# Optimization experiments

Hardware: AMD Instinct MI355X
Metric: run time of the kernel (lower is better)

## Reference

```python
import jax, jax.numpy as jnp
import numpy as np

WIN = (2, 4, 4)
SHIFT = (1, 2, 2)
NUM_HEADS = 8
LN_EPS = 1e-5


def _rel_pos_index(ws):
    wt, wh, ww = ws
    coords = np.stack(np.meshgrid(np.arange(wt), np.arange(wh), np.arange(ww), indexing='ij'))
    cf = coords.reshape(3, -1)                      # [3, N]
    rel = cf[:, :, None] - cf[:, None, :]           # [3, N, N]
    rel = rel.transpose(1, 2, 0).copy()             # [N, N, 3]
    rel[..., 0] += wt - 1
    rel[..., 1] += wh - 1
    rel[..., 2] += ww - 1
    rel[..., 0] *= (2 * wh - 1) * (2 * ww - 1)
    rel[..., 1] *= 2 * ww - 1
    return rel.sum(-1)                              # [N, N] int

REL_IDX = _rel_pos_index(WIN)


def _layer_norm(x, w, b):
    mu = jnp.mean(x, axis=-1, keepdims=True)
    var = jnp.mean(jnp.square(x - mu), axis=-1, keepdims=True)
    return (x - mu) * jax.lax.rsqrt(var + LN_EPS) * w + b


def setup_inputs() -> dict:
    key = jax.random.key(0)
    ks = jax.random.split(key, 8)
    C, Cm = 256, 1024
    inp = {
        'x': jax.random.normal(ks[0], (2, 16, 64, 64, C), jnp.float32),
        'norm1_w': jnp.ones((C,), jnp.float32),
        'norm1_b': jnp.zeros((C,), jnp.float32),
        'qkv_w': jax.random.normal(ks[1], (C, 3 * C), jnp.float32) * 0.02,
        'qkv_b': jnp.zeros((3 * C,), jnp.float32),
        'proj_w': jax.random.normal(ks[2], (C, C), jnp.float32) * 0.02,
        'proj_b': jnp.zeros((C,), jnp.float32),
        'rel_bias_table': jax.random.normal(ks[3], (147, NUM_HEADS), jnp.float32) * 0.02,
        'norm2_w': jnp.ones((C,), jnp.float32),
        'norm2_b': jnp.zeros((C,), jnp.float32),
        'mlp_w1': jax.random.normal(ks[4], (C, Cm), jnp.float32) * 0.02,
        'mlp_b1': jnp.zeros((Cm,), jnp.float32),
        'mlp_w2': jax.random.normal(ks[5], (Cm, C), jnp.float32) * 0.02,
        'mlp_b2': jnp.zeros((C,), jnp.float32),
    }
    return inp


def reference(x, norm1_w, norm1_b, qkv_w, qkv_b, proj_w, proj_b,
              rel_bias_table, norm2_w, norm2_b, mlp_w1, mlp_b1, mlp_w2, mlp_b2):
    B, T, H, W, C = x.shape
    wT, wH, wW = WIN
    nh = NUM_HEADS
    d = C // nh
    scale = d ** (-0.5)
    N = wT * wH * wW

    shortcut = x
    h = _layer_norm(x, norm1_w, norm1_b)
    # cyclic shift (no attention mask is applied in the original block)
    h = jnp.roll(h, shift=(-SHIFT[0], -SHIFT[1], -SHIFT[2]), axis=(1, 2, 3))
    # window partition -> [B*nW, N, C]
    h = h.reshape(B, T // wT, wT, H // wH, wH, W // wW, wW, C)
    h = h.transpose(0, 1, 3, 5, 2, 4, 6, 7).reshape(-1, N, C)
    B_ = h.shape[0]

    qkv = (h @ qkv_w + qkv_b).reshape(B_, N, 3, nh, d).transpose(2, 0, 3, 1, 4)
    q, k, v = qkv[0] * scale, qkv[1], qkv[2]          # [B_, nh, N, d]
    attn = jnp.einsum('bhnd,bhmd->bhnm', q, k)        # [B_, nh, N, N]
    bias = rel_bias_table[REL_IDX].transpose(2, 0, 1)  # [nh, N, N]
    attn = jax.nn.softmax(attn + bias[None], axis=-1)
    o = jnp.einsum('bhnm,bhmd->bhnd', attn, v)
    o = o.transpose(0, 2, 1, 3).reshape(B_, N, C)
    o = o @ proj_w + proj_b

    # window reverse -> [B, T, H, W, C]
    o = o.reshape(B, T // wT, H // wH, W // wW, wT, wH, wW, C)
    o = o.transpose(0, 1, 4, 2, 5, 3, 6, 7).reshape(B, T, H, W, C)
    o = jnp.roll(o, shift=SHIFT, axis=(1, 2, 3))

    x = shortcut + o
    m = _layer_norm(x, norm2_w, norm2_b)
    m = jax.nn.gelu(m @ mlp_w1 + mlp_b1, approximate=False) @ mlp_w2 + mlp_b2
    return x + m
```

## Files before the change

### kernel.cpp

```cpp
#include <hip/hip_runtime.h>
#include <hip/hip_bf16.h>
#include <cstdint>
#include <cstddef>

typedef __attribute__((ext_vector_type(8)))  short  s16x8;
typedef __attribute__((ext_vector_type(4)))  float  fp32x4;
typedef __attribute__((ext_vector_type(16))) float  fp32x16;
typedef __attribute__((ext_vector_type(4)))  unsigned short u16x4;

static __device__ __forceinline__ float bf2f(unsigned short u) {
    union { unsigned int i; float f; } v; v.i = ((unsigned int)u) << 16; return v.f;
}
static __device__ __forceinline__ unsigned short f2bf(float f) {
    __hip_bfloat16 h = __float2bfloat16(f);
    return __builtin_bit_cast(unsigned short, h);
}

static __device__ __forceinline__ fp32x16 mfma32(s16x8 a, s16x8 b, fp32x16 c) {
    return __builtin_amdgcn_mfma_f32_32x32x16_bf16(a, b, c, 0, 0, 0);
}
static __device__ __forceinline__ fp32x4 mfma16(s16x8 a, s16x8 b, fp32x4 c) {
    return __builtin_amdgcn_mfma_f32_16x16x32_bf16(a, b, c, 0, 0, 0);
}

static __device__ __forceinline__ float wave_sum(float v) {
#pragma unroll
    for (int off = 32; off > 0; off >>= 1) v += __shfl_xor(v, off, 64);
    return v;
}

#define NTOK   131072
#define CDIM   256

__global__ void prep_kernel(const float* __restrict__ qkv_w, const float* __restrict__ proj_w,
                            const float* __restrict__ w1,    const float* __restrict__ w2,
                            const float* __restrict__ rel,
                            unsigned short* __restrict__ qkvT, unsigned short* __restrict__ projT,
                            unsigned short* __restrict__ w1T,  unsigned short* __restrict__ w2T,
                            float* __restrict__ btab) {
    int id = blockIdx.x * 256 + threadIdx.x;
    if (id < 196608) {
        int n = id >> 8, k = id & 255;
        qkvT[id] = f2bf(qkv_w[k * 768 + n]);
    } else if (id < 262144) {
        int e = id - 196608; int n = e >> 8, k = e & 255;
        projT[e] = f2bf(proj_w[k * 256 + n]);
    } else if (id < 524288) {
        int e = id - 262144; int n = e >> 8, k = e & 255;
        w1T[e] = f2bf(w1[k * 1024 + n]);
    } else if (id < 786432) {
        int e = id - 524288; int n = e >> 10, k = e & 1023;
        w2T[e] = f2bf(w2[k * 256 + n]);
    } else {
        int e = id - 786432;
        int h = e >> 10, rem = e & 1023, n = rem >> 5, m = rem & 31;
        int tn = n >> 4, hn = (n >> 2) & 3, wn = n & 3;
        int tm = m >> 4, hm = (m >> 2) & 3, wm = m & 3;
        int ridx = (tn - tm + 1) * 49 + (hn - hm + 3) * 7 + (wn - wm + 3);
        btab[e] = rel[ridx * 8 + h];
    }
}

template <int MODE>
__global__ __launch_bounds__(256) void ln_kernel(const float* __restrict__ in,
                                                 const float* __restrict__ w,
                                                 const float* __restrict__ b,
                                                 unsigned short* __restrict__ out) {
    int tid = threadIdx.x, lane = tid & 63, wid = tid >> 6;
    long r = (long)blockIdx.x * 4 + wid;
    long src;
    if (MODE == 0) {
        int n = (int)(r & 31); int win = (int)(r >> 5);
        int b_ = win >> 11, tw = (win >> 8) & 7, hw = (win >> 4) & 15, ww = win & 15;
        int ti = n >> 4, hi = (n >> 2) & 3, wi = n & 3;
        int t = tw * 2 + ti, hh = hw * 4 + hi, wv = ww * 4 + wi;
        int ts = (t + 1) & 15, hs = (hh + 2) & 63, wsd = (wv + 2) & 63;
        src = ((long)((b_ * 16 + ts) * 64 + hs)) * 64 + wsd;
    } else {
        src = r;
    }
    float4 v = *(const float4*)&in[src * CDIM + lane * 4];
    float vv[4] = {v.x, v.y, v.z, v.w};
    float s = vv[0] + vv[1] + vv[2] + vv[3];
    s = wave_sum(s);
    float mean = s * (1.0f / 256.0f);
    float q = vv[0]*vv[0] + vv[1]*vv[1] + vv[2]*vv[2] + vv[3]*vv[3];
    q = wave_sum(q);
    float var = q * (1.0f / 256.0f) - mean * mean;
    float rstd = rsqrtf(var + 1e-5f);
    int c0 = lane * 4;
    u16x4 o;
#pragma unroll
    for (int j = 0; j < 4; ++j)
        o[j] = f2bf((vv[j] - mean) * rstd * w[c0 + j] + b[c0 + j]);
    *(u16x4*)&out[r * CDIM + c0] = o;
}

template <int K, int EPI, int NS, int NX>
__global__ __launch_bounds__(512) void gemm256(const unsigned short* __restrict__ A,
                                               const unsigned short* __restrict__ Bt,
                                               const float* __restrict__ bias,
                                               float* __restrict__ outf,
                                               unsigned short* __restrict__ outb,
                                               const float* __restrict__ resid) {
    extern __shared__ unsigned short lds[];
    const int tid = threadIdx.x;
    const int lane = tid & 63, wid = tid >> 6;
    const int wm = wid >> 2, wn = wid & 3;
    constexpr int NWG = NX * 512;
    constexpr int CPX = NWG / 8;
    const int bid = blockIdx.x;
    const int wg = (bid & 7) * CPX + (bid >> 3);
    const int n0 = (wg % NX) * 256;
    const size_t m0 = (size_t)(wg / NX) * 256;
    constexpr int NK = K / 64;

    fp32x4 acc[8][4] = {};

    auto stage = [&](int kt, int buf) {
#pragma unroll
        for (int i = 0; i < 4; ++i) {
            int L = i * 512 + tid;
            int r = L >> 3, c = L & 7;
            int sc = c ^ (r & 7);
            const unsigned short* ga = A + (m0 + r) * K + kt * 64 + sc * 8;
            __builtin_amdgcn_global_load_lds(
                (const __attribute__((address_space(1))) void*)ga,
                (__attribute__((address_space(3))) void*)(lds + buf * 16384 + L * 8),
                16, 0, 0);
            const unsigned short* gb = Bt + (size_t)(n0 + r) * K + kt * 64 + sc * 8;
            __builtin_amdgcn_global_load_lds(
                (const __attribute__((address_space(1))) void*)gb,
                (__attribute__((address_space(3))) void*)(lds + 32768 + buf * 16384 + L * 8),
                16, 0, 0);
        }
    };

    stage(0, 0);
    __syncthreads();
    for (int kt = 0; kt < NK; ++kt) {
        if (kt + 1 < NK) stage(kt + 1, (kt + 1) & 1);
        const unsigned short* As = lds + (kt & 1) * 16384;
        const unsigned short* Bs = lds + 32768 + (kt & 1) * 16384;
#pragma unroll
        for (int q = 0; q < 4; ++q) {
            const int qm = q >> 1, qn = q & 1;
            s16x8 a[4][2], b[2][2];
#pragma unroll
            for (int m = 0; m < 4; ++m)
#pragma unroll
                for (int ks = 0; ks < 2; ++ks) {
                    int row = wm * 128 + qm * 64 + m * 16 + (lane & 15);
                    int j = ks * 4 + (lane >> 4);
                    a[m][ks] = *(const s16x8*)(As + row * 64 + ((j ^ (row & 7)) << 3));
                }
#pragma unroll
            for (int n = 0; n < 2; ++n)
#pragma unroll
                for (int ks = 0; ks < 2; ++ks) {
                    int row = wn * 64 + qn * 32 + n * 16 + (lane & 15);
                    int j = ks * 4 + (lane >> 4);
                    b[n][ks] = *(const s16x8*)(Bs + row * 64 + ((j ^ (row & 7)) << 3));
                }
#pragma unroll
            for (int ks = 0; ks < 2; ++ks)
#pragma unroll
                for (int m = 0; m < 4; ++m)
#pragma unroll
                    for (int n = 0; n < 2; ++n)
                        acc[qm * 4 + m][qn * 2 + n] =
                            mfma16(a[m][ks], b[n][ks], acc[qm * 4 + m][qn * 2 + n]);
        }
        __syncthreads();
    }

    float bv[4];
#pragma unroll
    for (int n = 0; n < 4; ++n) bv[n] = bias[n0 + wn * 64 + n * 16 + (lane & 15)];

#pragma unroll
    for (int m = 0; m < 8; ++m) {
#pragma unroll
        for (int rg = 0; rg < 4; ++rg) {
            int row_t = wm * 128 + m * 16 + ((lane >> 4) << 2) + rg;
            size_t gr = m0 + row_t;
            size_t dst = 0;
            if (EPI == 1) {
                int win = (int)(gr >> 5), n_ = (int)(gr & 31);
                int b_ = win >> 11, tw = (win >> 8) & 7, hw = (win >> 4) & 15, ww = win & 15;
                int ti = n_ >> 4, hi = (n_ >> 2) & 3, wi = n_ & 3;
                int t = tw * 2 + ti, hh = hw * 4 + hi, wv = ww * 4 + wi;
                int ts = (t + 1) & 15, hs = (hh + 2) & 63, wsd = (wv + 2) & 63;
                dst = ((size_t)((b_ * 16 + ts) * 64 + hs)) * 64 + wsd;
            }
#pragma unroll
            for (int n = 0; n < 4; ++n) {
                int gc = n0 + wn * 64 + n * 16 + (lane & 15);
                float v = acc[m][n][rg] + bv[n];
                if (EPI == 0) {
                    outb[gr * NS + gc] = f2bf(v);
                } else if (EPI == 1) {
                    outf[dst * CDIM + gc] = resid[dst * CDIM + gc] + v;
                } else if (EPI == 2) {
                    float g = 0.5f * v * (1.0f + erff(v * 0.70710678118654752f));
                    outb[gr * NS + gc] = f2bf(g);
                } else {
                    outf[gr * NS + gc] += v;
                }
            }
        }
    }
}

__global__ __launch_bounds__(256) void attn_kernel(const unsigned short* __restrict__ qkv,
                                                   const float* __restrict__ btab,
                                                   unsigned short* __restrict__ obuf) {
    __shared__ unsigned short sP[4][1280];
    __shared__ unsigned short sVt[4][1280];
    int tid = threadIdx.x, lane = tid & 63, wid = tid >> 6;
    int task = blockIdx.x * 4 + wid;
    int win = task >> 3, hh = task & 7;
    const unsigned short* base = qkv + (size_t)win * 32 * 768 + hh * 32;
    int q = lane & 31, h = lane >> 5;

    s16x8 v0 = *(const s16x8*)(base + 512 + q * 768 + h * 16);
    s16x8 v1 = *(const s16x8*)(base + 512 + q * 768 + h * 16 + 8);
#pragma unroll
    for (int j = 0; j < 8; ++j) {
        sVt[wid][(h * 16 + j) * 40 + q]     = (unsigned short)v0[j];
        sVt[wid][(h * 16 + 8 + j) * 40 + q] = (unsigned short)v1[j];
    }

    s16x8 aq0 = *(const s16x8*)(base + q * 768 + h * 8);
    s16x8 aq1 = *(const s16x8*)(base + q * 768 + 16 + h * 8);
    s16x8 bk0 = *(const s16x8*)(base + 256 + q * 768 + h * 8);
    s16x8 bk1 = *(const s16x8*)(base + 256 + q * 768 + 16 + h * 8);
    fp32x16 S = {0.0f};
    S = mfma32(aq0, bk0, S);
    S = mfma32(aq1, bk1, S);

    const float scale = 0.17677669529663687f;
    float pr[16];
#pragma unroll
    for (int r = 0; r < 16; ++r) {
        int row = (r & 3) + 8 * (r >> 2) + 4 * h;
        float bvv = btab[(hh * 32 + row) * 32 + q];
        pr[r] = S[r] * scale + bvv;
    }
#pragma unroll
    for (int r = 0; r < 16; ++r) {
        float mx = pr[r];
#pragma unroll
        for (int off = 16; off > 0; off >>= 1) mx = fmaxf(mx, __shfl_xor(mx, off, 64));
        float e = __expf(pr[r] - mx);
        float sm = e;
#pragma unroll
        for (int off = 16; off > 0; off >>= 1) sm += __shfl_xor(sm, off, 64);
        pr[r] = e * __builtin_amdgcn_rcpf(sm);
    }
#pragma unroll
    for (int r = 0; r < 16; ++r) {
        int row = (r & 3) + 8 * (r >> 2) + 4 * h;
        sP[wid][row * 40 + q] = f2bf(pr[r]);
    }
    __syncthreads();

    s16x8 pa0 = *(const s16x8*)&sP[wid][q * 40 + h * 8];
    s16x8 pa1 = *(const s16x8*)&sP[wid][q * 40 + 16 + h * 8];
    s16x8 vb0 = *(const s16x8*)&sVt[wid][q * 40 + h * 8];
    s16x8 vb1 = *(const s16x8*)&sVt[wid][q * 40 + 16 + h * 8];
    fp32x16 O = {0.0f};
    O = mfma32(pa0, vb0, O);
    O = mfma32(pa1, vb1, O);
#pragma unroll
    for (int r = 0; r < 16; ++r) {
        int row = (r & 3) + 8 * (r >> 2) + 4 * h;
        obuf[((size_t)win * 32 + row) * 256 + hh * 32 + q] = f2bf(O[r]);
    }
}

extern "C" void kernel_launch(void* const* d_in, const int* in_sizes, int n_in,
                              void* d_out, int out_size, void* d_ws, size_t ws_size,
                              hipStream_t stream) {
    const float* x      = (const float*)d_in[0];
    const float* n1w    = (const float*)d_in[1];
    const float* n1b    = (const float*)d_in[2];
    const float* qkv_w  = (const float*)d_in[3];
    const float* qkv_b  = (const float*)d_in[4];
    const float* proj_w = (const float*)d_in[5];
    const float* proj_b = (const float*)d_in[6];
    const float* rel    = (const float*)d_in[7];
    const float* n2w    = (const float*)d_in[8];
    const float* n2b    = (const float*)d_in[9];
    const float* w1     = (const float*)d_in[10];
    const float* b1     = (const float*)d_in[11];
    const float* w2     = (const float*)d_in[12];
    const float* b2     = (const float*)d_in[13];
    float* out = (float*)d_out;

    char* ws = (char*)d_ws;
    unsigned short* hwin = (unsigned short*)ws;
    unsigned short* big  = (unsigned short*)(ws + 67108864);
    char* wreg = ws + 67108864 + 268435456;
    unsigned short* qkvT  = (unsigned short*)(wreg);
    unsigned short* projT = (unsigned short*)(wreg + 393216);
    unsigned short* w1T   = (unsigned short*)(wreg + 524288);
    unsigned short* w2T   = (unsigned short*)(wreg + 1048576);
    float*          btab  = (float*)(wreg + 1572864);

    prep_kernel<<<3104, 256, 0, stream>>>(qkv_w, proj_w, w1, w2, rel, qkvT, projT, w1T, w2T, btab);

    ln_kernel<0><<<NTOK / 4, 256, 0, stream>>>(x, n1w, n1b, hwin);

    gemm256<256, 0, 768, 3><<<1536, 512, 131072, stream>>>(hwin, qkvT, qkv_b, nullptr, big, nullptr);

    attn_kernel<<<8192, 256, 0, stream>>>(big, btab, hwin);

    gemm256<256, 1, 256, 1><<<512, 512, 131072, stream>>>(hwin, projT, proj_b, out, nullptr, x);

    ln_kernel<1><<<NTOK / 4, 256, 0, stream>>>(out, n2w, n2b, hwin);

    gemm256<256, 2, 1024, 4><<<2048, 512, 131072, stream>>>(hwin, w1T, b1, nullptr, big, nullptr);

    gemm256<1024, 3, 256, 1><<<512, 512, 131072, stream>>>(big, w2T, b2, out, nullptr, nullptr);
}
```

Before: 597.8 us.

## Fuse LayerNorm2 into projection GEMM epilogue and use tanh-form GELU

```diff
diff --git a/kernel.cpp b/kernel.cpp
--- a/kernel.cpp
+++ b/kernel.cpp
@@ -27,6 +27,11 @@
 #pragma unroll
     for (int off = 32; off > 0; off >>= 1) v += __shfl_xor(v, off, 64);
     return v;
+}
+
+static __device__ __forceinline__ float gelu_f(float u) {
+    float t = u * (1.0f + 0.044715f * u * u) * 1.595769122f;
+    return u * (1.0f / (1.0f + __expf(-t)));
 }
 
 #define NTOK   131072
@@ -61,24 +66,19 @@
     }
 }
 
-template <int MODE>
 __global__ __launch_bounds__(256) void ln_kernel(const float* __restrict__ in,
                                                  const float* __restrict__ w,
                                                  const float* __restrict__ b,
                                                  unsigned short* __restrict__ out) {
     int tid = threadIdx.x, lane = tid & 63, wid = tid >> 6;
     long r = (long)blockIdx.x * 4 + wid;
-    long src;
-    if (MODE == 0) {
-        int n = (int)(r & 31); int win = (int)(r >> 5);
-        int b_ = win >> 11, tw = (win >> 8) & 7, hw = (win >> 4) & 15, ww = win & 15;
-        int ti = n >> 4, hi = (n >> 2) & 3, wi = n & 3;
-        int t = tw * 2 + ti, hh = hw * 4 + hi, wv = ww * 4 + wi;
-        int ts = (t + 1) & 15, hs = (hh + 2) & 63, wsd = (wv + 2) & 63;
-        src = ((long)((b_ * 16 + ts) * 64 + hs)) * 64 + wsd;
-    } else {
-        src = r;
-    }
+    int n = (int)(r & 31); int win = (int)(r >> 5);
+    int b_ = win >> 11, tw = (win >> 8) & 7, hw = (win >> 4) & 15, ww = win & 15;
+    int ti = n >> 4, hi = (n >> 2) & 3, wi = n & 3;
+    int t = tw * 2 + ti, hh = hw * 4 + hi, wv = ww * 4 + wi;
+    int ts = (t + 1) & 15, hs = (hh + 2) & 63, wsd = (wv + 2) & 63;
+    long src = ((long)((b_ * 16 + ts) * 64 + hs)) * 64 + wsd;
+
     float4 v = *(const float4*)&in[src * CDIM + lane * 4];
     float vv[4] = {v.x, v.y, v.z, v.w};
     float s = vv[0] + vv[1] + vv[2] + vv[3];
@@ -102,7 +102,9 @@
                                                const float* __restrict__ bias,
                                                float* __restrict__ outf,
                                                unsigned short* __restrict__ outb,
-                                               const float* __restrict__ resid) {
+                                               const float* __restrict__ resid,
+                                               const float* __restrict__ lnw,
+                                               const float* __restrict__ lnb) {
     extern __shared__ unsigned short lds[];
     const int tid = threadIdx.x;
     const int lane = tid & 63, wid = tid >> 6;
@@ -143,33 +145,25 @@
         const unsigned short* As = lds + (kt & 1) * 16384;
         const unsigned short* Bs = lds + 32768 + (kt & 1) * 16384;
 #pragma unroll
-        for (int q = 0; q < 4; ++q) {
-            const int qm = q >> 1, qn = q & 1;
-            s16x8 a[4][2], b[2][2];
-#pragma unroll
-            for (int m = 0; m < 4; ++m)
-#pragma unroll
-                for (int ks = 0; ks < 2; ++ks) {
-                    int row = wm * 128 + qm * 64 + m * 16 + (lane & 15);
-                    int j = ks * 4 + (lane >> 4);
-                    a[m][ks] = *(const s16x8*)(As + row * 64 + ((j ^ (row & 7)) << 3));
-                }
-#pragma unroll
-            for (int n = 0; n < 2; ++n)
-#pragma unroll
-                for (int ks = 0; ks < 2; ++ks) {
-                    int row = wn * 64 + qn * 32 + n * 16 + (lane & 15);
-                    int j = ks * 4 + (lane >> 4);
-                    b[n][ks] = *(const s16x8*)(Bs + row * 64 + ((j ^ (row & 7)) << 3));
-                }
-#pragma unroll
-            for (int ks = 0; ks < 2; ++ks)
-#pragma unroll
-                for (int m = 0; m < 4; ++m)
-#pragma unroll
-                    for (int n = 0; n < 2; ++n)
-                        acc[qm * 4 + m][qn * 2 + n] =
-                            mfma16(a[m][ks], b[n][ks], acc[qm * 4 + m][qn * 2 + n]);
+        for (int ks = 0; ks < 2; ++ks) {
+            s16x8 a[8], b[4];
+#pragma unroll
+            for (int m = 0; m < 8; ++m) {
+                int row = wm * 128 + m * 16 + (lane & 15);
+                int j = ks * 4 + (lane >> 4);
+                a[m] = *(const s16x8*)(As + row * 64 + ((j ^ (row & 7)) << 3));
+            }
+#pragma unroll
+            for (int n = 0; n < 4; ++n) {
+                int row = wn * 64 + n * 16 + (lane & 15);
+                int j = ks * 4 + (lane >> 4);
+                b[n] = *(const s16x8*)(Bs + row * 64 + ((j ^ (row & 7)) << 3));
+            }
+#pragma unroll
+            for (int m = 0; m < 8; ++m)
+#pragma unroll
+                for (int n = 0; n < 4; ++n)
+                    acc[m][n] = mfma16(a[m], b[n], acc[m][n]);
         }
         __syncthreads();
     }
@@ -178,34 +172,92 @@
 #pragma unroll
     for (int n = 0; n < 4; ++n) bv[n] = bias[n0 + wn * 64 + n * 16 + (lane & 15)];
 
-#pragma unroll
-    for (int m = 0; m < 8; ++m) {
-#pragma unroll
-        for (int rg = 0; rg < 4; ++rg) {
-            int row_t = wm * 128 + m * 16 + ((lane >> 4) << 2) + rg;
-            size_t gr = m0 + row_t;
-            size_t dst = 0;
-            if (EPI == 1) {
+    if (EPI == 1) {
+        float* part = (float*)lds;
+        float lw[4], lb[4];
+#pragma unroll
+        for (int n = 0; n < 4; ++n) {
+            int gc = wn * 64 + n * 16 + (lane & 15);
+            lw[n] = lnw[gc]; lb[n] = lnb[gc];
+        }
+#pragma unroll
+        for (int m = 0; m < 8; ++m) {
+#pragma unroll
+            for (int rg = 0; rg < 4; ++rg) {
+                int row_t = wm * 128 + m * 16 + ((lane >> 4) << 2) + rg;
+                size_t gr = m0 + row_t;
                 int win = (int)(gr >> 5), n_ = (int)(gr & 31);
                 int b_ = win >> 11, tw = (win >> 8) & 7, hw = (win >> 4) & 15, ww = win & 15;
                 int ti = n_ >> 4, hi = (n_ >> 2) & 3, wi = n_ & 3;
                 int t = tw * 2 + ti, hh = hw * 4 + hi, wv = ww * 4 + wi;
                 int ts = (t + 1) & 15, hs = (hh + 2) & 63, wsd = (wv + 2) & 63;
-                dst = ((size_t)((b_ * 16 + ts) * 64 + hs)) * 64 + wsd;
-            }
-#pragma unroll
-            for (int n = 0; n < 4; ++n) {
-                int gc = n0 + wn * 64 + n * 16 + (lane & 15);
-                float v = acc[m][n][rg] + bv[n];
-                if (EPI == 0) {
-                    outb[gr * NS + gc] = f2bf(v);
-                } else if (EPI == 1) {
-                    outf[dst * CDIM + gc] = resid[dst * CDIM + gc] + v;
-                } else if (EPI == 2) {
-                    float g = 0.5f * v * (1.0f + erff(v * 0.70710678118654752f));
-                    outb[gr * NS + gc] = f2bf(g);
-                } else {
-                    outf[gr * NS + gc] += v;
+                size_t dst = ((size_t)((b_ * 16 + ts) * 64 + hs)) * 64 + wsd;
+                float s = 0.f, q = 0.f;
+#pragma unroll
+                for (int n = 0; n < 4; ++n) {
+                    int gc = wn * 64 + n * 16 + (lane & 15);
+                    float v = acc[m][n][rg] + bv[n] + resid[dst * CDIM + gc];
+                    outf[dst * CDIM + gc] = v;
+                    acc[m][n][rg] = v;
+                    s += v; q += v * v;
+                }
+#pragma unroll
+                for (int off = 1; off < 16; off <<= 1) {
+                    s += __shfl_xor(s, off, 16);
+                    q += __shfl_xor(q, off, 16);
+                }
+                if ((lane & 15) == 0) {
+                    part[(row_t * 4 + wn) * 2]     = s;
+                    part[(row_t * 4 + wn) * 2 + 1] = q;
+                }
+            }
+        }
+        __syncthreads();
+#pragma unroll
+        for (int m = 0; m < 8; ++m) {
+#pragma unroll
+            for (int rg = 0; rg < 4; ++rg) {
+                int row_t = wm * 128 + m * 16 + ((lane >> 4) << 2) + rg;
+                size_t gr = m0 + row_t;
+                int win = (int)(gr >> 5), n_ = (int)(gr & 31);
+                int b_ = win >> 11, tw = (win >> 8) & 7, hw = (win >> 4) & 15, ww = win & 15;
+                int ti = n_ >> 4, hi = (n_ >> 2) & 3, wi = n_ & 3;
+                int t = tw * 2 + ti, hh = hw * 4 + hi, wv = ww * 4 + wi;
+                int ts = (t + 1) & 15, hs = (hh + 2) & 63, wsd = (wv + 2) & 63;
+                size_t dst = ((size_t)((b_ * 16 + ts) * 64 + hs)) * 64 + wsd;
+                float4 p0 = *(const float4*)&part[row_t * 8];
+                float4 p1 = *(const float4*)&part[row_t * 8 + 4];
+                float s = p0.x + p0.z + p1.x + p1.z;
+                float q = p0.y + p0.w + p1.y + p1.w;
+                float mean = s * (1.0f / 256.0f);
+                float var  = q * (1.0f / 256.0f) - mean * mean;
+                float rstd = rsqrtf(var + 1e-5f);
+#pragma unroll
+                for (int n = 0; n < 4; ++n) {
+                    int gc = wn * 64 + n * 16 + (lane & 15);
+                    float v = acc[m][n][rg];
+                    outb[dst * CDIM + gc] = f2bf((v - mean) * rstd * lw[n] + lb[n]);
+                }
+            }
+        }
+    } else {
+#pragma unroll
+        for (int m = 0; m < 8; ++m) {
+#pragma unroll
+            for (int rg = 0; rg < 4; ++rg) {
+                int row_t = wm * 128 + m * 16 + ((lane >> 4) << 2) + rg;
+                size_t gr = m0 + row_t;
+#pragma unroll
+                for (int n = 0; n < 4; ++n) {
+                    int gc = n0 + wn * 64 + n * 16 + (lane & 15);
+                    float v = acc[m][n][rg] + bv[n];
+                    if (EPI == 0) {
+                        outb[gr * NS + gc] = f2bf(v);
+                    } else if (EPI == 2) {
+                        outb[gr * NS + gc] = f2bf(gelu_f(v));
+                    } else {
+                        outf[gr * NS + gc] += v;
+                    }
                 }
             }
         }
@@ -301,6 +353,7 @@
     char* ws = (char*)d_ws;
     unsigned short* hwin = (unsigned short*)ws;
     unsigned short* big  = (unsigned short*)(ws + 67108864);
+    unsigned short* obuf = big + 100663296;
     char* wreg = ws + 67108864 + 268435456;
     unsigned short* qkvT  = (unsigned short*)(wreg);
     unsigned short* projT = (unsigned short*)(wreg + 393216);
@@ -310,17 +363,19 @@
 
     prep_kernel<<<3104, 256, 0, stream>>>(qkv_w, proj_w, w1, w2, rel, qkvT, projT, w1T, w2T, btab);
 
-    ln_kernel<0><<<NTOK / 4, 256, 0, stream>>>(x, n1w, n1b, hwin);
-
-    gemm256<256, 0, 768, 3><<<1536, 512, 131072, stream>>>(hwin, qkvT, qkv_b, nullptr, big, nullptr);
-
-    attn_kernel<<<8192, 256, 0, stream>>>(big, btab, hwin);
-
-    gemm256<256, 1, 256, 1><<<512, 512, 131072, stream>>>(hwin, projT, proj_b, out, nullptr, x);
-
-    ln_kernel<1><<<NTOK / 4, 256, 0, stream>>>(out, n2w, n2b, hwin);
-
-    gemm256<256, 2, 1024, 4><<<2048, 512, 131072, stream>>>(hwin, w1T, b1, nullptr, big, nullptr);
-
-    gemm256<1024, 3, 256, 1><<<512, 512, 131072, stream>>>(big, w2T, b2, out, nullptr, nullptr);
-}
+    ln_kernel<<<NTOK / 4, 256, 0, stream>>>(x, n1w, n1b, hwin);
+
+    gemm256<256, 0, 768, 3><<<1536, 512, 131072, stream>>>(hwin, qkvT, qkv_b, nullptr, big,
+                                                           nullptr, nullptr, nullptr);
+
+    attn_kernel<<<8192, 256, 0, stream>>>(big, btab, obuf);
+
+    gemm256<256, 1, 256, 1><<<512, 512, 131072, stream>>>(obuf, projT, proj_b, out, hwin,
+                                                          x, n2w, n2b);
+
+    gemm256<256, 2, 1024, 4><<<2048, 512, 131072, stream>>>(hwin, w1T, b1, nullptr, big,
+                                                            nullptr, nullptr, nullptr);
+
+    gemm256<1024, 3, 256, 1><<<512, 512, 131072, stream>>>(big, w2T, b2, out, nullptr,
+                                                           nullptr, nullptr, nullptr);
+}
```

Measured after the change: 653.1 us. 9.2% more time.
